# Optimization experiments

Measured on AMD Instinct MI355X. Metric: run time of the kernel, lower is better.

The kernel has to match this reference:

```python
import jax, jax.numpy as jnp
import numpy as np

NUM_HEADS = 12
FEATURE_DIM = 16
HEAD_DIM = 128
EPS = 1e-12


def taylor_map(x):
    # x: [b, h, t, d] -> [b, h, t, 1 + d + d*d] (2nd-order Taylor features of exp)
    d = x.shape[-1]
    r2 = jnp.asarray(np.sqrt(2.0), x.dtype)
    rd = jnp.asarray(np.sqrt(d), x.dtype)
    rrd = jnp.asarray(np.sqrt(np.sqrt(d)), x.dtype)
    x2 = (x[..., :, None] * x[..., None, :]).reshape(x.shape[:-1] + (d * d,)) / r2
    ones = jnp.ones(x.shape[:-1] + (1,), x.dtype)
    return jnp.concatenate([ones, x / rrd, x2 / rd], axis=-1)


def setup_inputs() -> dict:
    key = jax.random.key(0)
    ks = jax.random.split(key, 5)
    b, t, hid = 2, 2048, 1536
    scale = 0.02
    return {
        "hidden_states": jax.random.normal(ks[0], (b, t, hid), jnp.float32),
        "Wq": jax.random.normal(ks[1], (NUM_HEADS * FEATURE_DIM, hid), jnp.float32) * scale,
        "Wk": jax.random.normal(ks[2], (NUM_HEADS * FEATURE_DIM, hid), jnp.float32) * scale,
        "Wv": jax.random.normal(ks[3], (NUM_HEADS * HEAD_DIM, hid), jnp.float32) * scale,
        "Wo": jax.random.normal(ks[4], (hid, NUM_HEADS * HEAD_DIM), jnp.float32) * scale,
    }


def reference(hidden_states, Wq, Wk, Wv, Wo):
    b, t, _ = hidden_states.shape
    H, dk, dv = NUM_HEADS, FEATURE_DIM, HEAD_DIM
    # projections (torch Linear: x @ W^T), split heads -> [b, h, t, d]
    q = (hidden_states @ Wq.T).reshape(b, t, H, dk).transpose(0, 2, 1, 3)
    k = (hidden_states @ Wk.T).reshape(b, t, H, dk).transpose(0, 2, 1, 3)
    v = (hidden_states @ Wv.T).reshape(b, t, H, dv).transpose(0, 2, 1, 3)
    qf = taylor_map(q)  # [b, h, t, D], D = 1 + dk + dk^2
    kf = taylor_map(k)
    # causal kernelized attention: identical math to cumsum-of-outer-products form
    S = jnp.einsum("bhtd,bhsd->bhts", qf, kf)  # [b, h, t, t]
    mask = jnp.tril(jnp.ones((t, t), bool))
    S = jnp.where(mask, S, jnp.zeros((), S.dtype))
    num = jnp.einsum("bhts,bhse->bhte", S, v)  # [b, h, t, dv]
    den = S.sum(-1) + EPS  # [b, h, t]
    y = num / den[..., None]
    y = y.transpose(0, 2, 1, 3).reshape(b, t, H * dv)
    return y @ Wo.T
```

## Files before the change

kernel.cpp:

```cpp
#include <hip/hip_runtime.h>

#define B 2
#define T 2048
#define HID 1536
#define NH 12
#define DK 16
#define DV 128
#define BT (B * T)
#define EPS 1e-12f

typedef __attribute__((ext_vector_type(8))) short bf16x8;
typedef __attribute__((ext_vector_type(4))) float f32x4;

__device__ __forceinline__ unsigned short f2bf(float f) {
    unsigned int u = __float_as_uint(f);
    u += 0x7FFFu + ((u >> 16) & 1u);
    return (unsigned short)(u >> 16);
}

__global__ __launch_bounds__(256) void cvt_all(const float* __restrict__ hs,
                                               const float* __restrict__ Wq,
                                               const float* __restrict__ Wk,
                                               const float* __restrict__ Wv,
                                               const float* __restrict__ Wo,
                                               unsigned short* __restrict__ hsb,
                                               unsigned short* __restrict__ wqk,
                                               unsigned short* __restrict__ wvb,
                                               unsigned short* __restrict__ wob) {
    int bx = blockIdx.x;
    const float* src;
    unsigned short* dst;
    if (bx < 3072)      { src = hs; dst = hsb; }
    else if (bx < 3216) { src = Wq; dst = wqk;          bx -= 3072; }
    else if (bx < 3360) { src = Wk; dst = wqk + 294912; bx -= 3216; }
    else if (bx < 4512) { src = Wv; dst = wvb;          bx -= 3360; }
    else                { src = Wo; dst = wob;          bx -= 4512; }
    const int i = (bx * 256 + threadIdx.x) * 8;
    float4 a = *(const float4*)(src + i);
    float4 b = *(const float4*)(src + i + 4);
    *(ushort4*)(dst + i)     = make_ushort4(f2bf(a.x), f2bf(a.y), f2bf(a.z), f2bf(a.w));
    *(ushort4*)(dst + i + 4) = make_ushort4(f2bf(b.x), f2bf(b.y), f2bf(b.z), f2bf(b.w));
}

template <int MODE>
__global__ __launch_bounds__(256) void gemm_bf16_nt(const unsigned short* __restrict__ A,
                                                    const unsigned short* __restrict__ Bm,
                                                    void* __restrict__ Cv,
                                                    int M, int N, int K) {
    __shared__ unsigned short As[128 * 32];
    __shared__ unsigned short Bs[128 * 32];
    const int tid = threadIdx.x;
    const int m0 = blockIdx.y * 128;
    const int n0 = blockIdx.x * 128;
    const int wave = tid >> 6, lane = tid & 63;
    const int wm = (wave & 1) * 64, wn = (wave >> 1) * 64;
    const int fr = lane & 15;
    const int fk = (lane >> 4) * 8;

    f32x4 acc[4][4];
#pragma unroll
    for (int i = 0; i < 4; ++i)
#pragma unroll
        for (int j = 0; j < 4; ++j) acc[i][j] = (f32x4)0.f;

    const int c0 = tid, c1 = tid + 256;
    const int r0 = c0 >> 2, q0 = (c0 & 3) * 8;
    const int r1 = c1 >> 2, q1 = (c1 & 3) * 8;

    for (int k0 = 0; k0 < K; k0 += 32) {
        __builtin_amdgcn_global_load_lds(
            (const __attribute__((address_space(1))) void*)(A + (size_t)(m0 + r0) * K + k0 + q0),
            (__attribute__((address_space(3))) void*)(As + c0 * 8), 16, 0, 0);
        __builtin_amdgcn_global_load_lds(
            (const __attribute__((address_space(1))) void*)(A + (size_t)(m0 + r1) * K + k0 + q1),
            (__attribute__((address_space(3))) void*)(As + c1 * 8), 16, 0, 0);
        __builtin_amdgcn_global_load_lds(
            (const __attribute__((address_space(1))) void*)(Bm + (size_t)(n0 + r0) * K + k0 + q0),
            (__attribute__((address_space(3))) void*)(Bs + c0 * 8), 16, 0, 0);
        __builtin_amdgcn_global_load_lds(
            (const __attribute__((address_space(1))) void*)(Bm + (size_t)(n0 + r1) * K + k0 + q1),
            (__attribute__((address_space(3))) void*)(Bs + c1 * 8), 16, 0, 0);
        __syncthreads();

        bf16x8 af[4], bfr[4];
#pragma unroll
        for (int mb = 0; mb < 4; ++mb)
            af[mb] = *(const bf16x8*)(As + (wm + mb * 16 + fr) * 32 + fk);
#pragma unroll
        for (int nb = 0; nb < 4; ++nb)
            bfr[nb] = *(const bf16x8*)(Bs + (wn + nb * 16 + fr) * 32 + fk);
#pragma unroll
        for (int mb = 0; mb < 4; ++mb)
#pragma unroll
            for (int nb = 0; nb < 4; ++nb)
                acc[mb][nb] = __builtin_amdgcn_mfma_f32_16x16x32_bf16(
                    af[mb], bfr[nb], acc[mb][nb], 0, 0, 0);
        __syncthreads();
    }

    const int orow = (lane >> 4) * 4;
#pragma unroll
    for (int nb = 0; nb < 4; ++nb) {
        const int col = n0 + wn + nb * 16 + fr;
#pragma unroll
        for (int mb = 0; mb < 4; ++mb) {
            const int row = m0 + wm + mb * 16 + orow;
            if (MODE == 0) {
                float* C = (float*)Cv;
#pragma unroll
                for (int r = 0; r < 4; ++r)
                    C[(size_t)(row + r) * N + col] = acc[mb][nb][r];
            } else {
                unsigned short* C = (unsigned short*)Cv;
#pragma unroll
                for (int r = 0; r < 4; ++r)
                    C[(size_t)(row + r) * N + col] = f2bf(acc[mb][nb][r]);
            }
        }
    }
}

__global__ __launch_bounds__(256) void based_attn_mfma(const unsigned short* __restrict__ qk,
                                                       const unsigned short* __restrict__ vt,
                                                       unsigned short* __restrict__ yb) {
    const int bx = blockIdx.x;
    const int qt = (T / 64 - 1) - (bx / (NH * B));
    const int hb = bx % (NH * B);
    const int h  = hb >> 1;
    const int bi = hb & 1;
    const int tid = threadIdx.x;
    const int wave = tid >> 6, lane = tid & 63;
    const int fr = lane & 15, quad = lane >> 4;
    const int fk = quad * 8;

    __shared__ __attribute__((aligned(16))) unsigned short ss[2][64][72];
    __shared__ float den_lds[64];
    if (tid < 64) den_lds[tid] = 0.f;

    const bf16x8 zf = {};
    bf16x8 qf[4];
#pragma unroll
    for (int nt = 0; nt < 4; ++nt) {
        qf[nt] = zf;
        if (quad < 2)
            qf[nt] = *(const bf16x8*)&qk[(size_t)(bi * T + qt * 64 + nt * 16 + fr) * 384
                                         + h * DK + fk];
    }

    f32x4 oacc[2][4];
#pragma unroll
    for (int mt = 0; mt < 2; ++mt)
#pragma unroll
        for (int nt = 0; nt < 4; ++nt) oacc[mt][nt] = (f32x4)0.f;
    float denp[4] = {0.f, 0.f, 0.f, 0.f};

    for (int kt = 0; kt <= qt; ++kt) {
        const int bsel = kt & 1;
        bf16x8 kf = zf;
        if (quad < 2)
            kf = *(const bf16x8*)&qk[(size_t)(bi * T + kt * 64 + wave * 16 + fr) * 384
                                     + 192 + h * DK + fk];
        bf16x8 vf[2][2];
#pragma unroll
        for (int mt = 0; mt < 2; ++mt)
#pragma unroll
            for (int k2 = 0; k2 < 2; ++k2)
                vf[mt][k2] = *(const bf16x8*)&vt[(size_t)(h * DV + wave * 32 + mt * 16 + fr) * BT
                                                 + bi * T + kt * 64 + k2 * 32 + fk];
        f32x4 sa[4];
#pragma unroll
        for (int nt = 0; nt < 4; ++nt)
            sa[nt] = __builtin_amdgcn_mfma_f32_16x16x32_bf16(kf, qf[nt], (f32x4)0.f, 0, 0, 0);

        const bool diag = (kt == qt);
#pragma unroll
        for (int nt = 0; nt < 4; ++nt) {
            const int i = nt * 16 + fr;
            float sv[4];
#pragma unroll
            for (int r = 0; r < 4; ++r) {
                const int j = wave * 16 + quad * 4 + r;
                const float a = sa[nt][r];
                float s = 1.f + 0.25f * a + a * a * (1.f / 32.f);
                if (diag && (j > i)) s = 0.f;
                sv[r] = s;
                denp[nt] += s;
            }
            *(ushort4*)&ss[bsel][i][wave * 16 + quad * 4] =
                make_ushort4(f2bf(sv[0]), f2bf(sv[1]), f2bf(sv[2]), f2bf(sv[3]));
        }
        __syncthreads();

#pragma unroll
        for (int k2 = 0; k2 < 2; ++k2) {
            bf16x8 sf[4];
#pragma unroll
            for (int nt = 0; nt < 4; ++nt)
                sf[nt] = *(const bf16x8*)&ss[bsel][nt * 16 + fr][k2 * 32 + fk];
#pragma unroll
            for (int mt = 0; mt < 2; ++mt)
#pragma unroll
                for (int nt = 0; nt < 4; ++nt)
                    oacc[mt][nt] = __builtin_amdgcn_mfma_f32_16x16x32_bf16(
                        vf[mt][k2], sf[nt], oacc[mt][nt], 0, 0, 0);
        }
    }

#pragma unroll
    for (int nt = 0; nt < 4; ++nt) {
        float v = denp[nt];
        v += __shfl_xor(v, 16);
        v += __shfl_xor(v, 32);
        if (quad == 0) atomicAdd(&den_lds[nt * 16 + fr], v);
    }
    __syncthreads();

#pragma unroll
    for (int nt = 0; nt < 4; ++nt) {
        const int i = nt * 16 + fr;
        const float rd = 1.f / (den_lds[i] + EPS);
        const size_t rowbase = (size_t)(bi * T + qt * 64 + i) * (NH * DV) + h * DV;
#pragma unroll
        for (int mt = 0; mt < 2; ++mt) {
            const int c = wave * 32 + mt * 16 + quad * 4;
            const f32x4 o = oacc[mt][nt];
            *(ushort4*)&yb[rowbase + c] = make_ushort4(f2bf(o[0] * rd), f2bf(o[1] * rd),
                                                       f2bf(o[2] * rd), f2bf(o[3] * rd));
        }
    }
}

extern "C" void kernel_launch(void* const* d_in, const int* in_sizes, int n_in,
                              void* d_out, int out_size, void* d_ws, size_t ws_size,
                              hipStream_t stream) {
    (void)in_sizes; (void)n_in; (void)out_size; (void)ws_size;
    const float* hs = (const float*)d_in[0];
    const float* Wq = (const float*)d_in[1];
    const float* Wk = (const float*)d_in[2];
    const float* Wv = (const float*)d_in[3];
    const float* Wo = (const float*)d_in[4];
    float* out = (float*)d_out;

    unsigned short* hsb = (unsigned short*)d_ws;
    unsigned short* wqk = hsb + (size_t)BT * HID;
    unsigned short* wvb = wqk + (size_t)384 * HID;
    unsigned short* wob = wvb + (size_t)HID * HID;
    unsigned short* qkb = wob + (size_t)HID * HID;
    unsigned short* vtg = qkb + (size_t)BT * 384;
    unsigned short* ybb = vtg + (size_t)HID * BT;

    dim3 blk(256);
    cvt_all<<<dim3(5664), blk, 0, stream>>>(hs, Wq, Wk, Wv, Wo, hsb, wqk, wvb, wob);

    gemm_bf16_nt<1><<<dim3(3, 32), blk, 0, stream>>>(hsb, wqk, qkb, BT, 384, HID);
    gemm_bf16_nt<1><<<dim3(32, 12), blk, 0, stream>>>(wvb, hsb, vtg, HID, BT, HID);

    based_attn_mfma<<<dim3(T / 64 * NH * B), blk, 0, stream>>>(qkb, vtg, ybb);

    gemm_bf16_nt<0><<<dim3(12, 32), blk, 0, stream>>>(ybb, wob, out, BT, HID, HID);
}
```

Measured before the change: 256.1 us.

## Merge QK and V projections into one launch and split attention over value halves

Combines the QK projection GEMM and the transposed V projection GEMM into a single kernel with 480 blocks. V tiles are grouped so neighbouring blocks share hidden-state columns. The attention kernel now splits the 128-wide value dimension into two halves, doubling the grid to 1536 blocks and halving per-block accumulators. This removes a launch and improves occupancy and load balance for the causal attention. In exchange, the score matrix (QK^T and the Taylor map) is computed twice per tile, once per value half. The output GEMM is specialized with constant dimensions.

```diff
diff --git a/kernel.cpp b/kernel.cpp
--- a/kernel.cpp
+++ b/kernel.cpp
@@ -42,11 +42,93 @@
     *(ushort4*)(dst + i + 4) = make_ushort4(f2bf(b.x), f2bf(b.y), f2bf(b.z), f2bf(b.w));
 }
 
-template <int MODE>
-__global__ __launch_bounds__(256) void gemm_bf16_nt(const unsigned short* __restrict__ A,
-                                                    const unsigned short* __restrict__ Bm,
-                                                    void* __restrict__ Cv,
-                                                    int M, int N, int K) {
+__device__ __forceinline__ void gemm_tile_bf16(const unsigned short* __restrict__ A,
+                                               const unsigned short* __restrict__ Bm,
+                                               unsigned short* __restrict__ C,
+                                               int m0, int n0, int K, int ldc,
+                                               unsigned short* As, unsigned short* Bs) {
+    const int tid = threadIdx.x;
+    const int wave = tid >> 6, lane = tid & 63;
+    const int wm = (wave & 1) * 64, wn = (wave >> 1) * 64;
+    const int fr = lane & 15;
+    const int fk = (lane >> 4) * 8;
+
+    f32x4 acc[4][4];
+#pragma unroll
+    for (int i = 0; i < 4; ++i)
+#pragma unroll
+        for (int j = 0; j < 4; ++j) acc[i][j] = (f32x4)0.f;
+
+    const int c0 = tid, c1 = tid + 256;
+    const int r0 = c0 >> 2, q0 = (c0 & 3) * 8;
+    const int r1 = c1 >> 2, q1 = (c1 & 3) * 8;
+
+    for (int k0 = 0; k0 < K; k0 += 32) {
+        __builtin_amdgcn_global_load_lds(
+            (const __attribute__((address_space(1))) void*)(A + (size_t)(m0 + r0) * K + k0 + q0),
+            (__attribute__((address_space(3))) void*)(As + c0 * 8), 16, 0, 0);
+        __builtin_amdgcn_global_load_lds(
+            (const __attribute__((address_space(1))) void*)(A + (size_t)(m0 + r1) * K + k0 + q1),
+            (__attribute__((address_space(3))) void*)(As + c1 * 8), 16, 0, 0);
+        __builtin_amdgcn_global_load_lds(
+            (const __attribute__((address_space(1))) void*)(Bm + (size_t)(n0 + r0) * K + k0 + q0),
+            (__attribute__((address_space(3))) void*)(Bs + c0 * 8), 16, 0, 0);
+        __builtin_amdgcn_global_load_lds(
+            (const __attribute__((address_space(1))) void*)(Bm + (size_t)(n0 + r1) * K + k0 + q1),
+            (__attribute__((address_space(3))) void*)(Bs + c1 * 8), 16, 0, 0);
+        __syncthreads();
+
+        bf16x8 af[4], bfr[4];
+#pragma unroll
+        for (int mb = 0; mb < 4; ++mb)
+            af[mb] = *(const bf16x8*)(As + (wm + mb * 16 + fr) * 32 + fk);
+#pragma unroll
+        for (int nb = 0; nb < 4; ++nb)
+            bfr[nb] = *(const bf16x8*)(Bs + (wn + nb * 16 + fr) * 32 + fk);
+#pragma unroll
+        for (int mb = 0; mb < 4; ++mb)
+#pragma unroll
+            for (int nb = 0; nb < 4; ++nb)
+                acc[mb][nb] = __builtin_amdgcn_mfma_f32_16x16x32_bf16(
+                    af[mb], bfr[nb], acc[mb][nb], 0, 0, 0);
+        __syncthreads();
+    }
+
+    const int orow = (lane >> 4) * 4;
+#pragma unroll
+    for (int nb = 0; nb < 4; ++nb) {
+        const int col = n0 + wn + nb * 16 + fr;
+#pragma unroll
+        for (int mb = 0; mb < 4; ++mb) {
+            const int row = m0 + wm + mb * 16 + orow;
+#pragma unroll
+            for (int r = 0; r < 4; ++r)
+                C[(size_t)(row + r) * ldc + col] = f2bf(acc[mb][nb][r]);
+        }
+    }
+}
+
+__global__ __launch_bounds__(256) void proj_qkv(const unsigned short* __restrict__ hsb,
+                                                const unsigned short* __restrict__ wqk,
+                                                const unsigned short* __restrict__ wvb,
+                                                unsigned short* __restrict__ qkb,
+                                                unsigned short* __restrict__ vtg) {
+    __shared__ unsigned short As[128 * 32];
+    __shared__ unsigned short Bs[128 * 32];
+    const int bx = blockIdx.x;
+    if (bx < 96) {
+        gemm_tile_bf16(hsb, wqk, qkb, (bx / 3) * 128, (bx % 3) * 128, HID, 384, As, Bs);
+    } else {
+        const int vid = bx - 96;
+        const int grp = vid / 48, sub = vid % 48;
+        const int n_t = grp * 4 + (sub & 3), m_t = sub >> 2;
+        gemm_tile_bf16(wvb, hsb, vtg, m_t * 128, n_t * 128, HID, BT, As, Bs);
+    }
+}
+
+__global__ __launch_bounds__(256) void proj_out(const unsigned short* __restrict__ A,
+                                                const unsigned short* __restrict__ Bm,
+                                                float* __restrict__ C) {
     __shared__ unsigned short As[128 * 32];
     __shared__ unsigned short Bs[128 * 32];
     const int tid = threadIdx.x;
@@ -56,6 +138,7 @@
     const int wm = (wave & 1) * 64, wn = (wave >> 1) * 64;
     const int fr = lane & 15;
     const int fk = (lane >> 4) * 8;
+    const int K = HID;
 
     f32x4 acc[4][4];
 #pragma unroll
@@ -105,17 +188,9 @@
 #pragma unroll
         for (int mb = 0; mb < 4; ++mb) {
             const int row = m0 + wm + mb * 16 + orow;
-            if (MODE == 0) {
-                float* C = (float*)Cv;
-#pragma unroll
-                for (int r = 0; r < 4; ++r)
-                    C[(size_t)(row + r) * N + col] = acc[mb][nb][r];
-            } else {
-                unsigned short* C = (unsigned short*)Cv;
-#pragma unroll
-                for (int r = 0; r < 4; ++r)
-                    C[(size_t)(row + r) * N + col] = f2bf(acc[mb][nb][r]);
-            }
+#pragma unroll
+            for (int r = 0; r < 4; ++r)
+                C[(size_t)(row + r) * HID + col] = acc[mb][nb][r];
         }
     }
 }
@@ -124,10 +199,11 @@
                                                        const unsigned short* __restrict__ vt,
                                                        unsigned short* __restrict__ yb) {
     const int bx = blockIdx.x;
-    const int qt = (T / 64 - 1) - (bx / (NH * B));
-    const int hb = bx % (NH * B);
-    const int h  = hb >> 1;
-    const int bi = hb & 1;
+    const int qt = (T / 64 - 1) - (bx / (NH * B * 2));
+    const int sub = bx % (NH * B * 2);
+    const int h   = sub >> 2;
+    const int bi  = (sub >> 1) & 1;
+    const int dvs = sub & 1;
     const int tid = threadIdx.x;
     const int wave = tid >> 6, lane = tid & 63;
     const int fr = lane & 15, quad = lane >> 4;
@@ -147,12 +223,12 @@
                                          + h * DK + fk];
     }
 
-    f32x4 oacc[2][4];
-#pragma unroll
-    for (int mt = 0; mt < 2; ++mt)
-#pragma unroll
-        for (int nt = 0; nt < 4; ++nt) oacc[mt][nt] = (f32x4)0.f;
+    f32x4 oacc[4];
+#pragma unroll
+    for (int nt = 0; nt < 4; ++nt) oacc[nt] = (f32x4)0.f;
     float denp[4] = {0.f, 0.f, 0.f, 0.f};
+
+    const size_t vrow = (size_t)(h * DV + dvs * 64 + wave * 16 + fr) * BT + bi * T;
 
     for (int kt = 0; kt <= qt; ++kt) {
         const int bsel = kt & 1;
@@ -160,13 +236,11 @@
         if (quad < 2)
             kf = *(const bf16x8*)&qk[(size_t)(bi * T + kt * 64 + wave * 16 + fr) * 384
                                      + 192 + h * DK + fk];
-        bf16x8 vf[2][2];
-#pragma unroll
-        for (int mt = 0; mt < 2; ++mt)
-#pragma unroll
-            for (int k2 = 0; k2 < 2; ++k2)
-                vf[mt][k2] = *(const bf16x8*)&vt[(size_t)(h * DV + wave * 32 + mt * 16 + fr) * BT
-                                                 + bi * T + kt * 64 + k2 * 32 + fk];
+        bf16x8 vf[2];
+#pragma unroll
+        for (int k2 = 0; k2 < 2; ++k2)
+            vf[k2] = *(const bf16x8*)&vt[vrow + kt * 64 + k2 * 32 + fk];
+
         f32x4 sa[4];
 #pragma unroll
         for (int nt = 0; nt < 4; ++nt)
@@ -198,11 +272,9 @@
             for (int nt = 0; nt < 4; ++nt)
                 sf[nt] = *(const bf16x8*)&ss[bsel][nt * 16 + fr][k2 * 32 + fk];
 #pragma unroll
-            for (int mt = 0; mt < 2; ++mt)
-#pragma unroll
-                for (int nt = 0; nt < 4; ++nt)
-                    oacc[mt][nt] = __builtin_amdgcn_mfma_f32_16x16x32_bf16(
-                        vf[mt][k2], sf[nt], oacc[mt][nt], 0, 0, 0);
+            for (int nt = 0; nt < 4; ++nt)
+                oacc[nt] = __builtin_amdgcn_mfma_f32_16x16x32_bf16(
+                    vf[k2], sf[nt], oacc[nt], 0, 0, 0);
         }
     }
 
@@ -220,13 +292,10 @@
         const int i = nt * 16 + fr;
         const float rd = 1.f / (den_lds[i] + EPS);
         const size_t rowbase = (size_t)(bi * T + qt * 64 + i) * (NH * DV) + h * DV;
-#pragma unroll
-        for (int mt = 0; mt < 2; ++mt) {
-            const int c = wave * 32 + mt * 16 + quad * 4;
-            const f32x4 o = oacc[mt][nt];
-            *(ushort4*)&yb[rowbase + c] = make_ushort4(f2bf(o[0] * rd), f2bf(o[1] * rd),
-                                                       f2bf(o[2] * rd), f2bf(o[3] * rd));
-        }
+        const int c = dvs * 64 + wave * 16 + quad * 4;
+        const f32x4 o = oacc[nt];
+        *(ushort4*)&yb[rowbase + c] = make_ushort4(f2bf(o[0] * rd), f2bf(o[1] * rd),
+                                                   f2bf(o[2] * rd), f2bf(o[3] * rd));
     }
 }
 
@@ -252,10 +321,9 @@
     dim3 blk(256);
     cvt_all<<<dim3(5664), blk, 0, stream>>>(hs, Wq, Wk, Wv, Wo, hsb, wqk, wvb, wob);
 
-    gemm_bf16_nt<1><<<dim3(3, 32), blk, 0, stream>>>(hsb, wqk, qkb, BT, 384, HID);
-    gemm_bf16_nt<1><<<dim3(32, 12), blk, 0, stream>>>(wvb, hsb, vtg, HID, BT, HID);
-
-    based_attn_mfma<<<dim3(T / 64 * NH * B), blk, 0, stream>>>(qkb, vtg, ybb);
-
-    gemm_bf16_nt<0><<<dim3(12, 32), blk, 0, stream>>>(ybb, wob, out, BT, HID, HID);
-}
+    proj_qkv<<<dim3(480), blk, 0, stream>>>(hsb, wqk, wvb, qkb, vtg);
+
+    based_attn_mfma<<<dim3(T / 64 * NH * B * 2), blk, 0, stream>>>(qkb, vtg, ybb);
+
+    proj_out<<<dim3(12, 32), blk, 0, stream>>>(ybb, wob, out);
+}
```

Measured after the change: 216.4 us. 15.5% less time.
